# Performance work log

Hardware: AMD Instinct MI355X
Metric: run time of the kernel (lower is better)

## Reference

```python
import jax, jax.numpy as jnp
import numpy as np

B, S, H = 4, 2048, 1024

def setup_inputs() -> dict:
    key = jax.random.key(0)
    ks = jax.random.split(key, 6)
    scale = 1.0 / np.sqrt(H)
    return {
        "query": jax.random.normal(ks[0], (B, S, H), dtype=jnp.float32),
        "key":   jax.random.normal(ks[1], (B, S, H), dtype=jnp.float32),
        "value": jax.random.normal(ks[2], (B, S, H), dtype=jnp.float32),
        "Wq": jax.random.normal(ks[3], (H, H), dtype=jnp.float32) * scale,
        "Wk": jax.random.normal(ks[4], (H, H), dtype=jnp.float32) * scale,
        "Wv": jax.random.normal(ks[5], (H, H), dtype=jnp.float32) * scale,
    }

def reference(query, key, value, Wq, Wk, Wv):
    # nn.Linear(bias=False): y = x @ W.T
    q = jnp.einsum('bsh,oh->bso', query, Wq)
    k = jnp.einsum('bsh,oh->bso', key, Wk)
    v = jnp.einsum('bsh,oh->bso', value, Wv)
    # full QK^T scores [B, Q, K], scaled by sqrt(hidden_size)
    scores = jnp.einsum('bqh,bkh->bqk', q, k) / jnp.sqrt(jnp.asarray(H, q.dtype))
    attn = jax.nn.softmax(scores, axis=2)
    return jnp.einsum('bqk,bkh->bqh', attn, v)
```

## Files before the change

kernel.cpp:

```cpp
#include <hip/hip_runtime.h>
#include <hip/hip_bf16.h>
#include <stdint.h>

#define BATCH 4
#define SLEN  2048
#define HID   1024

typedef __attribute__((ext_vector_type(8))) short bfrag8;
typedef __attribute__((ext_vector_type(4))) float facc4;
typedef __attribute__((ext_vector_type(4))) unsigned short us4;

__device__ __forceinline__ float b2f(unsigned short u) {
  union { unsigned int i; float f; } x; x.i = ((unsigned int)u) << 16; return x.f;
}
__device__ __forceinline__ unsigned short f2b(float f) {
  union { float f; unsigned int i; } x; x.f = f;
  unsigned int r = x.i + 0x7FFFu + ((x.i >> 16) & 1u);
  return (unsigned short)(r >> 16);
}

__device__ __forceinline__ void gl_lds16(const void* g, void* l) {
  __builtin_amdgcn_global_load_lds(
      (const __attribute__((address_space(1))) void*)g,
      (__attribute__((address_space(3))) void*)l, 16, 0, 0);
}

__global__ __launch_bounds__(256) void cast_all(
    const float* __restrict__ q, const float* __restrict__ k,
    const float* __restrict__ v, const float* __restrict__ wq,
    const float* __restrict__ wk, const float* __restrict__ wv,
    us4* __restrict__ dst, float* __restrict__ lsum) {
  if (blockIdx.x < 8) {
    float4 z = {0.f, 0.f, 0.f, 0.f};
    ((float4*)lsum)[blockIdx.x * 256 + threadIdx.x] = z;
  }
  const long i = (long)blockIdx.x * 256 + threadIdx.x;
  const long S1 = 2097152, S2 = 4194304, S3 = 6291456,
             S4 = 6553600, S5 = 6815744;
  const float4* src; long off;
  if (i < S2) {
    if (i < S1) { src = (const float4*)q;  off = i; }
    else        { src = (const float4*)k;  off = i - S1; }
  } else if (i < S3) { src = (const float4*)v;  off = i - S2; }
  else if   (i < S4) { src = (const float4*)wq; off = i - S3; }
  else if   (i < S5) { src = (const float4*)wk; off = i - S4; }
  else               { src = (const float4*)wv; off = i - S5; }
  float4 x = src[off];
  us4 o;
  o.x = f2b(x.x); o.y = f2b(x.y); o.z = f2b(x.z); o.w = f2b(x.w);
  dst[i] = o;
}

template <int MODE, typename OutT>
__global__ __launch_bounds__(256) void gemm_nt(
    const unsigned short* __restrict__ A, const unsigned short* __restrict__ B,
    OutT* __restrict__ C, int K, int lda, int ldb, int ldc,
    long aStrideZ, long bStrideZ, long cStrideZ, float alpha,
    float* __restrict__ lsum) {
  A += (long)blockIdx.z * aStrideZ;
  B += (long)blockIdx.z * bStrideZ;
  C += (long)blockIdx.z * cStrideZ;
  const long lz = (long)blockIdx.z * SLEN;

  const int nbm = gridDim.x, nbn = gridDim.y;
  const int nb  = nbm * nbn;
  const int pid = blockIdx.y * nbm + blockIdx.x;
  const int p2  = (pid & 7) * (nb >> 3) + (pid >> 3);
  const int GROUP = 4;
  const int gsize = GROUP * nbn;
  const int gid   = p2 / gsize;
  const int rem   = p2 - gid * gsize;
  const long bm = (long)(gid * GROUP + (rem & (GROUP - 1))) * 128;
  const long bn = (long)(rem >> 2) * 128;

  __shared__ __align__(16) unsigned short As[128 * 64];
  __shared__ __align__(16) unsigned short Bs[128 * 64];

  const int tid  = threadIdx.x;
  const int lane = tid & 63;
  const int wave = tid >> 6;
  const int wr   = (wave >> 1) * 64;
  const int wc   = (wave & 1) * 64;
  const int ln   = lane & 15;
  const int lq   = lane >> 4;
  const int swz  = ln & 7;

  facc4 acc[4][4] = {};

  const unsigned short* ap[4]; const unsigned short* bp[4];
  unsigned short* asd[4]; unsigned short* bsd[4];
#pragma unroll
  for (int j = 0; j < 4; ++j) {
    const int c   = j * 256 + tid;
    const int row = c >> 3;
    const int src = ((c & 7) ^ (row & 7)) * 8;
    ap[j]  = A + (bm + row) * (long)lda + src;
    bp[j]  = B + (bn + row) * (long)ldb + src;
    asd[j] = &As[c * 8];
    bsd[j] = &Bs[c * 8];
  }

  for (int k0 = 0; k0 < K; k0 += 64) {
#pragma unroll
    for (int j = 0; j < 4; ++j) { gl_lds16(ap[j], asd[j]); ap[j] += 64; }
#pragma unroll
    for (int j = 0; j < 4; ++j) { gl_lds16(bp[j], bsd[j]); bp[j] += 64; }
    __syncthreads();

#pragma unroll
    for (int kk = 0; kk < 2; ++kk) {
      bfrag8 af[4], bfr[4];
#pragma unroll
      for (int i = 0; i < 4; ++i)
        af[i] = *(const bfrag8*)&As[(wr + i * 16 + ln) * 64 + ((kk * 4 + lq) ^ swz) * 8];
#pragma unroll
      for (int j = 0; j < 4; ++j)
        bfr[j] = *(const bfrag8*)&Bs[(wc + j * 16 + ln) * 64 + ((kk * 4 + lq) ^ swz) * 8];
#pragma unroll
      for (int i = 0; i < 4; ++i)
#pragma unroll
        for (int j = 0; j < 4; ++j)
          acc[i][j] = __builtin_amdgcn_mfma_f32_16x16x32_bf16(af[i], bfr[j], acc[i][j], 0, 0, 0);
    }
    __syncthreads();
  }

  if constexpr (MODE == 0) {
#pragma unroll
    for (int i = 0; i < 4; ++i)
#pragma unroll
      for (int j = 0; j < 4; ++j) {
        const long m = bm + wr + i * 16 + lq * 4;
        const long n = bn + wc + j * 16 + ln;
#pragma unroll
        for (int r = 0; r < 4; ++r)
          C[(m + r) * (long)ldc + n] = (OutT)f2b(acc[i][j][r] * alpha);
      }
  } else if constexpr (MODE == 1) {
#pragma unroll
    for (int i = 0; i < 4; ++i) {
#pragma unroll
      for (int r = 0; r < 4; ++r) {
        const long m = bm + wr + i * 16 + lq * 4 + r;
        float rowsum = 0.f;
#pragma unroll
        for (int j = 0; j < 4; ++j) {
          const long n = bn + wc + j * 16 + ln;
          float e = __expf(acc[i][j][r] * alpha);
          C[m * (long)ldc + n] = (OutT)f2b(e);
          rowsum += e;
        }
        rowsum += __shfl_xor(rowsum, 1, 64);
        rowsum += __shfl_xor(rowsum, 2, 64);
        rowsum += __shfl_xor(rowsum, 4, 64);
        rowsum += __shfl_xor(rowsum, 8, 64);
        if (ln == 0) atomicAdd(&lsum[lz + m], rowsum);
      }
    }
  } else {
    float inv[16];
#pragma unroll
    for (int i = 0; i < 4; ++i)
#pragma unroll
      for (int r = 0; r < 4; ++r)
        inv[i * 4 + r] = 1.0f / lsum[lz + bm + wr + i * 16 + lq * 4 + r];
#pragma unroll
    for (int i = 0; i < 4; ++i)
#pragma unroll
      for (int j = 0; j < 4; ++j) {
        const long m = bm + wr + i * 16 + lq * 4;
        const long n = bn + wc + j * 16 + ln;
#pragma unroll
        for (int r = 0; r < 4; ++r)
          ((float*)C)[(m + r) * (long)ldc + n] = acc[i][j][r] * inv[i * 4 + r];
      }
  }
}

extern "C" void kernel_launch(void* const* d_in, const int* in_sizes, int n_in,
                              void* d_out, int out_size, void* d_ws, size_t ws_size,
                              hipStream_t stream) {
  const float* q_in = (const float*)d_in[0];
  const float* k_in = (const float*)d_in[1];
  const float* v_in = (const float*)d_in[2];
  const float* wq   = (const float*)d_in[3];
  const float* wk   = (const float*)d_in[4];
  const float* wv   = (const float*)d_in[5];
  float* out = (float*)d_out;

  const long NXH = (long)BATCH * SLEN * HID;
  const long NW  = (long)HID * HID;
  const long SH  = (long)SLEN * HID;
  const long SS  = (long)SLEN * SLEN;

  unsigned short* ws = (unsigned short*)d_ws;
  unsigned short* Xq  = ws;
  unsigned short* Xk  = Xq  + NXH;
  unsigned short* Xv  = Xk  + NXH;
  unsigned short* Wqb = Xv  + NXH;
  unsigned short* Wkb = Wqb + NW;
  unsigned short* Wvb = Wkb + NW;
  unsigned short* Qb  = Wvb + NW;
  unsigned short* Kb  = Qb  + NXH;
  unsigned short* Vt  = Kb  + NXH;
  float*          lsum = (float*)(Vt + NXH);
  unsigned short* P   = Xq;

  const dim3 blk(256);

  cast_all<<<dim3(27648), blk, 0, stream>>>(q_in, k_in, v_in, wq, wk, wv,
                                            (us4*)ws, lsum);

  gemm_nt<0, unsigned short><<<dim3(64, 8, 2), blk, 0, stream>>>(
      Xq, Wqb, Qb, HID, HID, HID, HID, NXH, NW, NXH, 1.0f, nullptr);
  gemm_nt<0, unsigned short><<<dim3(8, 64, 1), blk, 0, stream>>>(
      Wvb, Xv, Vt, HID, HID, HID, BATCH * SLEN, 0, 0, 0, 1.0f, nullptr);

  gemm_nt<1, unsigned short><<<dim3(16, 16, BATCH), blk, 0, stream>>>(
      Qb, Kb, P, HID, HID, HID, SLEN, SH, SH, SS, 0.03125f, lsum);

  gemm_nt<2, float><<<dim3(16, 8, BATCH), blk, 0, stream>>>(
      P, Vt, out, SLEN, SLEN, BATCH * SLEN, HID, SS, SLEN, SH, 1.0f, lsum);
}
```

Measured before the change: 317.8 us.

## Fuse fp32-to-bf16 cast into a single QKV projection GEMM kernel

Replaces the separate cast kernel and two projection GEMM launches with one kernel. It loads fp32 inputs and weights directly, packs them to bf16 in registers and stores them to LDS, then runs the MFMA loop, covering Q, K and transposed-V tiles in one grid. This removes the bf16 copies of inputs and weights from global memory and two launches. In exchange the direct LDS loads become register-staged loads, with no overlap and twice the global bytes per tile. Weights are now re-read and re-converted as fp32 by every tile, and the cast rounds half-up instead of to nearest-even.

```diff
diff --git a/kernel.cpp b/kernel.cpp
--- a/kernel.cpp
+++ b/kernel.cpp
@@ -8,16 +8,17 @@
 
 typedef __attribute__((ext_vector_type(8))) short bfrag8;
 typedef __attribute__((ext_vector_type(4))) float facc4;
-typedef __attribute__((ext_vector_type(4))) unsigned short us4;
-
-__device__ __forceinline__ float b2f(unsigned short u) {
-  union { unsigned int i; float f; } x; x.i = ((unsigned int)u) << 16; return x.f;
-}
+
 __device__ __forceinline__ unsigned short f2b(float f) {
   union { float f; unsigned int i; } x; x.f = f;
   unsigned int r = x.i + 0x7FFFu + ((x.i >> 16) & 1u);
   return (unsigned short)(r >> 16);
 }
+__device__ __forceinline__ unsigned int pk2(float a, float b) {
+  unsigned int ua = __float_as_uint(a) + 0x8000u;
+  unsigned int ub = __float_as_uint(b) + 0x8000u;
+  return (ua >> 16) | (ub & 0xFFFF0000u);
+}
 
 __device__ __forceinline__ void gl_lds16(const void* g, void* l) {
   __builtin_amdgcn_global_load_lds(
@@ -25,30 +26,110 @@
       (__attribute__((address_space(3))) void*)l, 16, 0, 0);
 }
 
-__global__ __launch_bounds__(256) void cast_all(
+__global__ __launch_bounds__(256) void qkv_proj(
     const float* __restrict__ q, const float* __restrict__ k,
     const float* __restrict__ v, const float* __restrict__ wq,
     const float* __restrict__ wk, const float* __restrict__ wv,
-    us4* __restrict__ dst, float* __restrict__ lsum) {
-  if (blockIdx.x < 8) {
+    unsigned short* __restrict__ Qb, unsigned short* __restrict__ Kb,
+    unsigned short* __restrict__ Vt, float* __restrict__ lsum) {
+  const int pid = blockIdx.x;
+  if (pid < 8) {
     float4 z = {0.f, 0.f, 0.f, 0.f};
-    ((float4*)lsum)[blockIdx.x * 256 + threadIdx.x] = z;
-  }
-  const long i = (long)blockIdx.x * 256 + threadIdx.x;
-  const long S1 = 2097152, S2 = 4194304, S3 = 6291456,
-             S4 = 6553600, S5 = 6815744;
-  const float4* src; long off;
-  if (i < S2) {
-    if (i < S1) { src = (const float4*)q;  off = i; }
-    else        { src = (const float4*)k;  off = i - S1; }
-  } else if (i < S3) { src = (const float4*)v;  off = i - S2; }
-  else if   (i < S4) { src = (const float4*)wq; off = i - S3; }
-  else if   (i < S5) { src = (const float4*)wk; off = i - S4; }
-  else               { src = (const float4*)wv; off = i - S5; }
-  float4 x = src[off];
-  us4 o;
-  o.x = f2b(x.x); o.y = f2b(x.y); o.z = f2b(x.z); o.w = f2b(x.w);
-  dst[i] = o;
+    ((float4*)lsum)[pid * 256 + threadIdx.x] = z;
+  }
+  const int p2     = (pid & 7) * 192 + (pid >> 3);
+  const int g      = p2 >> 9;
+  const int within = p2 & 511;
+
+  const float* A; const float* B; unsigned short* C;
+  long bm, bn; int ldc_;
+  if (g == 0)      { A = q;  B = wq; C = Qb; }
+  else if (g == 1) { A = k;  B = wk; C = Kb; }
+  else             { A = wv; B = v;  C = Vt; }
+  if (g < 2) {
+    const int gid = within >> 5, rem = within & 31;
+    bm = (long)(gid * 4 + (rem & 3)) * 128;
+    bn = (long)(rem >> 2) * 128;
+    ldc_ = 1024;
+  } else {
+    const int gid = within >> 8, rem = within & 255;
+    bm = (long)(gid * 4 + (rem & 3)) * 128;
+    bn = (long)(rem >> 2) * 128;
+    ldc_ = 8192;
+  }
+
+  __shared__ __align__(16) unsigned short As[128 * 64];
+  __shared__ __align__(16) unsigned short Bs[128 * 64];
+
+  const int tid  = threadIdx.x;
+  const int lane = tid & 63;
+  const int wave = tid >> 6;
+  const int wr   = (wave >> 1) * 64;
+  const int wc   = (wave & 1) * 64;
+  const int ln   = lane & 15;
+  const int lq   = lane >> 4;
+  const int swz  = ln & 7;
+
+  facc4 acc[4][4] = {};
+
+  const float* ap[4]; const float* bp[4];
+  unsigned short* asd[4]; unsigned short* bsd[4];
+#pragma unroll
+  for (int j = 0; j < 4; ++j) {
+    const int c   = j * 256 + tid;
+    const int row = c >> 3;
+    const int src = ((c & 7) ^ (row & 7)) * 8;
+    ap[j]  = A + (bm + row) * 1024 + src;
+    bp[j]  = B + (bn + row) * 1024 + src;
+    asd[j] = &As[c * 8];
+    bsd[j] = &Bs[c * 8];
+  }
+
+  for (int k0 = 0; k0 < 1024; k0 += 64) {
+#pragma unroll
+    for (int j = 0; j < 4; ++j) {
+      const float4* a4 = (const float4*)ap[j];
+      const float4* b4 = (const float4*)bp[j];
+      float4 xa0 = a4[0], xa1 = a4[1];
+      float4 xb0 = b4[0], xb1 = b4[1];
+      ap[j] += 64; bp[j] += 64;
+      uint4 wa = { pk2(xa0.x, xa0.y), pk2(xa0.z, xa0.w),
+                   pk2(xa1.x, xa1.y), pk2(xa1.z, xa1.w) };
+      uint4 wb = { pk2(xb0.x, xb0.y), pk2(xb0.z, xb0.w),
+                   pk2(xb1.x, xb1.y), pk2(xb1.z, xb1.w) };
+      *(uint4*)asd[j] = wa;
+      *(uint4*)bsd[j] = wb;
+    }
+    __syncthreads();
+
+#pragma unroll
+    for (int kk = 0; kk < 2; ++kk) {
+      bfrag8 af[4], bfr[4];
+#pragma unroll
+      for (int i = 0; i < 4; ++i)
+        af[i] = *(const bfrag8*)&As[(wr + i * 16 + ln) * 64 + ((kk * 4 + lq) ^ swz) * 8];
+#pragma unroll
+      for (int j = 0; j < 4; ++j)
+        bfr[j] = *(const bfrag8*)&Bs[(wc + j * 16 + ln) * 64 + ((kk * 4 + lq) ^ swz) * 8];
+#pragma unroll
+      for (int i = 0; i < 4; ++i)
+#pragma unroll
+        for (int j = 0; j < 4; ++j)
+          acc[i][j] = __builtin_amdgcn_mfma_f32_16x16x32_bf16(af[i], bfr[j], acc[i][j], 0, 0, 0);
+    }
+    __syncthreads();
+  }
+
+#pragma unroll
+  for (int i = 0; i < 4; ++i)
+#pragma unroll
+    for (int j = 0; j < 4; ++j) {
+      const long m = bm + wr + i * 16 + lq * 4;
+      const long n = bn + wc + j * 16 + ln;
+#pragma unroll
+      for (int r = 0; r < 4; ++r)
+        C[(m + r) * (long)ldc_ + n] = f2b(acc[i][j][r]);
+    }
 }
 
 template <int MODE, typename OutT>
@@ -125,18 +206,7 @@
     __syncthreads();
   }
 
-  if constexpr (MODE == 0) {
-#pragma unroll
-    for (int i = 0; i < 4; ++i)
-#pragma unroll
-      for (int j = 0; j < 4; ++j) {
-        const long m = bm + wr + i * 16 + lq * 4;
-        const long n = bn + wc + j * 16 + ln;
-#pragma unroll
-        for (int r = 0; r < 4; ++r)
-          C[(m + r) * (long)ldc + n] = (OutT)f2b(acc[i][j][r] * alpha);
-      }
-  } else if constexpr (MODE == 1) {
+  if constexpr (MODE == 1) {
 #pragma unroll
     for (int i = 0; i < 4; ++i) {
 #pragma unroll
@@ -189,32 +259,20 @@
   float* out = (float*)d_out;
 
   const long NXH = (long)BATCH * SLEN * HID;
-  const long NW  = (long)HID * HID;
   const long SH  = (long)SLEN * HID;
   const long SS  = (long)SLEN * SLEN;
 
-  unsigned short* ws = (unsigned short*)d_ws;
-  unsigned short* Xq  = ws;
-  unsigned short* Xk  = Xq  + NXH;
-  unsigned short* Xv  = Xk  + NXH;
-  unsigned short* Wqb = Xv  + NXH;
-  unsigned short* Wkb = Wqb + NW;
-  unsigned short* Wvb = Wkb + NW;
-  unsigned short* Qb  = Wvb + NW;
-  unsigned short* Kb  = Qb  + NXH;
-  unsigned short* Vt  = Kb  + NXH;
+  unsigned short* ws  = (unsigned short*)d_ws;
+  unsigned short* Qb  = ws;
+  unsigned short* Kb  = Qb + NXH;
+  unsigned short* Vt  = Kb + NXH;
   float*          lsum = (float*)(Vt + NXH);
-  unsigned short* P   = Xq;
+  unsigned short* P   = (unsigned short*)(lsum + 8192);
 
   const dim3 blk(256);
 
-  cast_all<<<dim3(27648), blk, 0, stream>>>(q_in, k_in, v_in, wq, wk, wv,
-                                            (us4*)ws, lsum);
-
-  gemm_nt<0, unsigned short><<<dim3(64, 8, 2), blk, 0, stream>>>(
-      Xq, Wqb, Qb, HID, HID, HID, HID, NXH, NW, NXH, 1.0f, nullptr);
-  gemm_nt<0, unsigned short><<<dim3(8, 64, 1), blk, 0, stream>>>(
-      Wvb, Xv, Vt, HID, HID, HID, BATCH * SLEN, 0, 0, 0, 1.0f, nullptr);
+  qkv_proj<<<dim3(1536), blk, 0, stream>>>(q_in, k_in, v_in, wq, wk, wv,
+                                           Qb, Kb, Vt, lsum);
 
   gemm_nt<1, unsigned short><<<dim3(16, 16, BATCH), blk, 0, stream>>>(
       Qb, Kb, P, HID, HID, HID, SLEN, SH, SH, SS, 0.03125f, lsum);
```

Result: slower. 329.2 us (+3.6%).
